# Kernel tuning notes

Hardware: AMD Instinct MI355X
Metric: run time of the kernel (lower is better)

## Reference

```python
import jax, jax.numpy as jnp
import numpy as np

N = 1024
DH = 64   # XH feature dim (<= DOUT)
DP = 32   # XP feature dim
DIN = 64  # input_dim (== output_dim, required by f_psi applied to vij)
DOUT = 64 # output_dim
BN_EPS = 1e-5
SIGMA = 0.1


def setup_inputs() -> dict:
    key = jax.random.key(0)
    ks = jax.random.split(key, 8)
    return {
        "XH": jax.random.normal(ks[0], (N, DH), dtype=jnp.float32),
        "XP": jax.random.normal(ks[1], (N, DP), dtype=jnp.float32),
        "XX": jax.random.normal(ks[2], (N, DIN), dtype=jnp.float32),
        "K": 16,
        # nn.Parameter weight/bias: normal(0, 0.01)
        "weight": 0.01 * jax.random.normal(ks[3], (DIN, DOUT), dtype=jnp.float32),
        "bias": 0.01 * jax.random.normal(ks[4], (DOUT,), dtype=jnp.float32),
        # f_psi Linear params (torch kaiming-uniform ~ small uniform)
        "psi_w": jax.random.uniform(ks[5], (DOUT, DIN), dtype=jnp.float32, minval=-1.0, maxval=1.0) / np.sqrt(DIN),
        "psi_b": jax.random.uniform(ks[6], (DOUT,), dtype=jnp.float32, minval=-1.0, maxval=1.0) / np.sqrt(DIN),
        # BatchNorm1d affine params
        "gamma": jnp.ones((DOUT,), dtype=jnp.float32),
        "beta": jnp.zeros((DOUT,), dtype=jnp.float32),
    }


def _pairwise_norm(X):
    # [N, N] matrix of L2 norms of row differences (as in torch.norm(X[:,None]-X, dim=2))
    return jnp.linalg.norm(X[:, None, :] - X[None, :, :], axis=2)


def _adjacency(XH, XP, K, sigma=SIGMA):
    eps = float(np.finfo(np.float64).eps)
    XHs = XH / (sigma + eps)
    WHo = _pairwise_norm(XHs)
    WH = jnp.exp(-((WHo - WHo.min()) / (WHo.max() - WHo.min())) / 2)
    Wlo = _pairwise_norm(XP)
    Wl = jnp.exp(-((Wlo - Wlo.min()) / (Wlo.max() - Wlo.min())))
    WW = WH + 0.2 * Wl
    _, idx = jax.lax.top_k(WW, K)                       # per-row top-K neighbors
    n = WW.shape[0]
    mask = jnp.zeros_like(WW).at[jnp.arange(n)[:, None], idx].set(1.0)
    mask = mask + mask.T                                # symmetrize
    # Original sets Adj=WW/WW=1 where mask!=0 and Adj=WW-WW=0 elsewhere -> binary adjacency
    return (mask > 0).astype(WW.dtype)


def reference(XH, XP, XX, K, weight, bias, psi_w, psi_b, gamma, beta):
    Adj = _adjacency(XH, XP, K)                         # [N, N], {0,1}
    x = XX @ weight                                     # [N, D]
    vi = x[None, :, :] * Adj[:, :, None]                # [N, N, D]: vi[i,j] = x[j]*Adj[i,j]
    vij = x[None, :, :] + vi                            # [N, N, D]
    # f_psi: Linear -> BatchNorm1d (training-mode batch stats) -> Sigmoid, over N*N rows
    h = jnp.einsum('ijd,ed->ije', vij, psi_w) + psi_b   # [N, N, D]
    mu = h.mean(axis=(0, 1))                            # [D]
    var = h.var(axis=(0, 1))                            # biased var, as torch BN
    att = jax.nn.sigmoid((h - mu) * jax.lax.rsqrt(var + BN_EPS) * gamma + beta)
    # self-loop attention forced to 1 on the diagonal
    eye = jnp.eye(x.shape[0], dtype=bool)[:, :, None]
    att = jnp.where(eye, jnp.float32(1.0), att)
    out = (att * vi).sum(axis=0) + bias                 # [N, D]
    return (out[:, :XH.shape[1]], XP, out)
```

## Files before the change

### kernel.cpp

```cpp
#include <hip/hip_runtime.h>
#include <cfloat>

#define NN 1024


__global__ __launch_bounds__(256) void gcn_transpose(const float* __restrict__ XH,
                                                     const float* __restrict__ XP,
                                                     float* __restrict__ XHT,
                                                     float* __restrict__ XPT) {
    const int b = blockIdx.x;
    const int j0 = b * 64;
    const int tid = threadIdx.x;
    __shared__ float th[64][65];
    __shared__ float tp[32][65];
#pragma unroll
    for (int it = 0; it < 16; ++it) {
        int idx = it * 256 + tid;
        int jl = idx >> 6, d = idx & 63;
        th[d][jl] = XH[(j0 + jl) * 64 + d];
    }
#pragma unroll
    for (int it = 0; it < 8; ++it) {
        int idx = it * 256 + tid;
        int jl = idx >> 5, d = idx & 31;
        tp[d][jl] = XP[(j0 + jl) * 32 + d];
    }
    __syncthreads();
#pragma unroll
    for (int it = 0; it < 16; ++it) {
        int idx = it * 256 + tid;
        int d = idx >> 6, jl = idx & 63;
        XHT[d * NN + j0 + jl] = th[d][jl];
    }
#pragma unroll
    for (int it = 0; it < 8; ++it) {
        int idx = it * 256 + tid;
        int d = idx >> 6, jl = idx & 63;
        XPT[d * NN + j0 + jl] = tp[d][jl];
    }
}

__global__ __launch_bounds__(256) void gcn_dist(const float* __restrict__ XH,
                                                const float* __restrict__ XP,
                                                const float* __restrict__ XHT,
                                                const float* __restrict__ XPT,
                                                unsigned* __restrict__ maxbits) {
    const int i0 = blockIdx.x * 4;
    const int tid = threadIdx.x;
    __shared__ float shi[4][64];
    __shared__ float spi[4][32];
    shi[tid >> 6][tid & 63] = XH[(i0 + (tid >> 6)) * 64 + (tid & 63)];
    if (tid < 128) spi[tid >> 5][tid & 31] = XP[(i0 + (tid >> 5)) * 32 + (tid & 31)];
    __syncthreads();
    const float4* XHTv = (const float4*)XHT;
    const float4* XPTv = (const float4*)XPT;
    float4 dh[4], dp[4];
#pragma unroll
    for (int r = 0; r < 4; ++r) { dh[r] = make_float4(0, 0, 0, 0); dp[r] = make_float4(0, 0, 0, 0); }
#pragma unroll 8
    for (int d = 0; d < 64; ++d) {
        float4 h = XHTv[d * 256 + tid];
#pragma unroll
        for (int r = 0; r < 4; ++r) {
            float s = shi[r][d];
            float tx = h.x - s, ty = h.y - s, tz = h.z - s, tw = h.w - s;
            dh[r].x += tx * tx; dh[r].y += ty * ty; dh[r].z += tz * tz; dh[r].w += tw * tw;
        }
    }
#pragma unroll 8
    for (int d = 0; d < 32; ++d) {
        float4 p = XPTv[d * 256 + tid];
#pragma unroll
        for (int r = 0; r < 4; ++r) {
            float s = spi[r][d];
            float tx = p.x - s, ty = p.y - s, tz = p.z - s, tw = p.w - s;
            dp[r].x += tx * tx; dp[r].y += ty * ty; dp[r].z += tz * tz; dp[r].w += tw * tw;
        }
    }
    float mh = 0.f, mp = 0.f;
#pragma unroll
    for (int r = 0; r < 4; ++r) {
        mh = fmaxf(mh, fmaxf(fmaxf(dh[r].x, dh[r].y), fmaxf(dh[r].z, dh[r].w)));
        mp = fmaxf(mp, fmaxf(fmaxf(dp[r].x, dp[r].y), fmaxf(dp[r].z, dp[r].w)));
    }
#pragma unroll
    for (int m = 1; m < 64; m <<= 1) {
        mh = fmaxf(mh, __shfl_xor(mh, m));
        mp = fmaxf(mp, __shfl_xor(mp, m));
    }
    __shared__ float wmx[4][2];
    if ((tid & 63) == 0) { wmx[tid >> 6][0] = mh; wmx[tid >> 6][1] = mp; }
    __syncthreads();
    if (tid == 0) {
        float a = fmaxf(fmaxf(wmx[0][0], wmx[1][0]), fmaxf(wmx[2][0], wmx[3][0]));
        float b = fmaxf(fmaxf(wmx[0][1], wmx[1][1]), fmaxf(wmx[2][1], wmx[3][1]));
        atomicMax(&maxbits[0], __float_as_uint(a));
        atomicMax(&maxbits[32], __float_as_uint(b));
    }
}

__global__ __launch_bounds__(256) void gcn_topk(const float* __restrict__ XH,
                                                const float* __restrict__ XP,
                                                const float* __restrict__ XHT,
                                                const float* __restrict__ XPT,
                                                const unsigned* __restrict__ maxbits,
                                                const int* __restrict__ kptr,
                                                unsigned char* __restrict__ mask,
                                                int* __restrict__ indeg) {
    const int i0 = blockIdx.x * 4;
    const int tid = threadIdx.x;
    const int w = tid >> 6;
    const int lane = tid & 63;
    const int i = i0 + w;
    __shared__ float shi[4][64];
    __shared__ float spi[4][32];
    shi[tid >> 6][tid & 63] = XH[(i0 + (tid >> 6)) * 64 + (tid & 63)];
    if (tid < 128) spi[tid >> 5][tid & 31] = XP[(i0 + (tid >> 5)) * 32 + (tid & 31)];
    __syncthreads();
    const float cH = -0.5f / sqrtf(__uint_as_float(maxbits[0]));
    const float cP = -1.0f / sqrtf(__uint_as_float(maxbits[32]));
    const float4* XHTv = (const float4*)XHT;
    const float4* XPTv = (const float4*)XPT;
    float ww[16];
#pragma unroll
    for (int s = 0; s < 4; ++s) {
        float4 dh = make_float4(0, 0, 0, 0), dp = make_float4(0, 0, 0, 0);
#pragma unroll 8
        for (int d = 0; d < 64; ++d) {
            float4 h = XHTv[d * 256 + s * 64 + lane];
            float c = shi[w][d];
            float tx = h.x - c, ty = h.y - c, tz = h.z - c, tw = h.w - c;
            dh.x += tx * tx; dh.y += ty * ty; dh.z += tz * tz; dh.w += tw * tw;
        }
#pragma unroll 8
        for (int d = 0; d < 32; ++d) {
            float4 p = XPTv[d * 256 + s * 64 + lane];
            float c = spi[w][d];
            float tx = p.x - c, ty = p.y - c, tz = p.z - c, tw = p.w - c;
            dp.x += tx * tx; dp.y += ty * ty; dp.z += tz * tz; dp.w += tw * tw;
        }
        ww[s * 4 + 0] = expf(sqrtf(dh.x) * cH) + 0.2f * expf(sqrtf(dp.x) * cP);
        ww[s * 4 + 1] = expf(sqrtf(dh.y) * cH) + 0.2f * expf(sqrtf(dp.y) * cP);
        ww[s * 4 + 2] = expf(sqrtf(dh.z) * cH) + 0.2f * expf(sqrtf(dp.z) * cP);
        ww[s * 4 + 3] = expf(sqrtf(dh.w) * cH) + 0.2f * expf(sqrtf(dp.w) * cP);
    }
    const int K = *kptr;
    int jsave = 0;
    for (int t = 0; t < K; ++t) {
        float bv = -FLT_MAX; int bj = NN;
#pragma unroll
        for (int v = 0; v < 16; ++v) {
            int j = ((v >> 2) << 8) | (lane << 2) | (v & 3);
            float val = ww[v];
            if (val > bv || (val == bv && j < bj)) { bv = val; bj = j; }
        }
#pragma unroll
        for (int m = 1; m < 64; m <<= 1) {
            float ov = __shfl_xor(bv, m);
            int oj = __shfl_xor(bj, m);
            if (ov > bv || (ov == bv && oj < bj)) { bv = ov; bj = oj; }
        }
        if ((int)lane == t) jsave = bj;
        if (((bj >> 2) & 63) == lane) {
            int slot = ((bj >> 8) << 2) | (bj & 3);
#pragma unroll
            for (int v = 0; v < 16; ++v)
                if (v == slot) ww[v] = -FLT_MAX;
        }
    }
    if (lane < K) {
        mask[(size_t)i * NN + jsave] = 1;
        atomicAdd(&indeg[jsave], 1);
    }
}

__global__ __launch_bounds__(256) void gcn_overlap(const unsigned char* __restrict__ mask,
                                                   int* __restrict__ overlap) {
    const int gid = blockIdx.x * 256 + threadIdx.x;
    const int i = gid >> 10, j = gid & 1023;
    if (mask[gid] && mask[(size_t)j * NN + i]) atomicAdd(&overlap[j], 1);
}

__global__ __launch_bounds__(256) void gcn_degree(const int* __restrict__ indeg,
                                                  const int* __restrict__ overlap,
                                                  const int* __restrict__ kptr,
                                                  int* __restrict__ cdeg) {
    const int j = blockIdx.x * 256 + threadIdx.x;
    if (j < NN) cdeg[j] = *kptr + indeg[j] - overlap[j];
}

__global__ __launch_bounds__(64) void gcn_xy(const float* __restrict__ XX,
                                             const float* __restrict__ W,
                                             const float* __restrict__ psi_w,
                                             float* __restrict__ x,
                                             float* __restrict__ y) {
    const int i = blockIdx.x;
    const int e = threadIdx.x;
    __shared__ float xin[64], xs[64];
    xin[e] = XX[i * 64 + e];
    __syncthreads();
    float acc = 0.f;
#pragma unroll
    for (int d = 0; d < 64; ++d) acc += xin[d] * W[d * 64 + e];
    xs[e] = acc;
    x[i * 64 + e] = acc;
    __syncthreads();
    float acc2 = 0.f;
    const float* pw = psi_w + e * 64;
#pragma unroll
    for (int d = 0; d < 64; ++d) acc2 += xs[d] * pw[d];
    y[i * 64 + e] = acc2;
}

__global__ __launch_bounds__(256) void gcn_mu(const float* __restrict__ y,
                                              const int* __restrict__ cdeg,
                                              const float* __restrict__ psi_b,
                                              float* __restrict__ mu) {
    const int e = blockIdx.x;
    const int tid = threadIdx.x;
    __shared__ double red[256];
    double s = 0.0;
    for (int j = tid; j < NN; j += 256)
        s += (double)(NN + cdeg[j]) * (double)y[j * 64 + e];
    red[tid] = s;
    __syncthreads();
    for (int k = 128; k > 0; k >>= 1) {
        if (tid < k) red[tid] += red[tid + k];
        __syncthreads();
    }
    if (tid == 0) mu[e] = (float)(red[0] / 1048576.0) + psi_b[e];
}

__global__ __launch_bounds__(256) void gcn_var(const float* __restrict__ y,
                                               const int* __restrict__ cdeg,
                                               const float* __restrict__ psi_b,
                                               const float* __restrict__ gamma,
                                               const float* __restrict__ mu,
                                               float* __restrict__ scale) {
    const int e = blockIdx.x;
    const int tid = threadIdx.x;
    __shared__ double red[256];
    const float m = mu[e], b = psi_b[e];
    double s = 0.0;
    for (int j = tid; j < NN; j += 256) {
        float t = y[j * 64 + e];
        float a1 = t + b - m;
        float a2 = 2.f * t + b - m;
        int cj = cdeg[j];
        s += (double)(NN - cj) * (double)a1 * (double)a1
           + (double)cj * (double)a2 * (double)a2;
    }
    red[tid] = s;
    __syncthreads();
    for (int k = 128; k > 0; k >>= 1) {
        if (tid < k) red[tid] += red[tid + k];
        __syncthreads();
    }
    if (tid == 0) {
        double var = red[0] / 1048576.0;
        scale[e] = (float)(1.0 / sqrt(var + 1e-5)) * gamma[e];
    }
}

__global__ __launch_bounds__(64) void gcn_out(const float* __restrict__ x,
                                              const float* __restrict__ y,
                                              const int* __restrict__ cdeg,
                                              const float* __restrict__ psi_b,
                                              const float* __restrict__ beta,
                                              const float* __restrict__ mu,
                                              const float* __restrict__ scale,
                                              const float* __restrict__ bias,
                                              const float* __restrict__ XP,
                                              float* __restrict__ out) {
    const int j = blockIdx.x;
    const int e = threadIdx.x;
    float t = y[j * 64 + e];
    float z = (2.f * t + psi_b[e] - mu[e]) * scale[e] + beta[e];
    float s = 1.f / (1.f + expf(-z));
    float val = x[j * 64 + e] * ((float)(cdeg[j] - 1) * s + 1.f) + bias[e];
    out[j * 64 + e] = val;
    out[98304 + j * 64 + e] = val;
    if (e < 32) out[65536 + j * 32 + e] = XP[j * 32 + e];
}

extern "C" void kernel_launch(void* const* d_in, const int* in_sizes, int n_in,
                              void* d_out, int out_size, void* d_ws, size_t ws_size,
                              hipStream_t stream) {
    const float* XH    = (const float*)d_in[0];
    const float* XP    = (const float*)d_in[1];
    const float* XX    = (const float*)d_in[2];
    const int*   Kp    = (const int*)d_in[3];
    const float* W     = (const float*)d_in[4];
    const float* bias  = (const float*)d_in[5];
    const float* psi_w = (const float*)d_in[6];
    const float* psi_b = (const float*)d_in[7];
    const float* gamma = (const float*)d_in[8];
    const float* beta  = (const float*)d_in[9];
    float* out = (float*)d_out;
    char* ws = (char*)d_ws;

    unsigned char* mask = (unsigned char*)ws;
    int* indeg        = (int*)(ws + 0x100000);
    int* overlap      = (int*)(ws + 0x101000);
    unsigned* maxbits = (unsigned*)(ws + 0x102000);
    int* cdeg         = (int*)(ws + 0x103000);
    float* mu         = (float*)(ws + 0x104000);
    float* scale      = (float*)(ws + 0x104100);
    float* x          = (float*)(ws + 0x200000);
    float* y          = (float*)(ws + 0x240000);
    float* XHT        = (float*)(ws + 0x280000);
    float* XPT        = (float*)(ws + 0x2C0000);

    hipMemsetAsync(ws, 0, 0x102200, stream);

    gcn_transpose<<<dim3(16), dim3(256), 0, stream>>>(XH, XP, XHT, XPT);
    gcn_dist<<<dim3(256), dim3(256), 0, stream>>>(XH, XP, XHT, XPT, maxbits);
    gcn_topk<<<dim3(256), dim3(256), 0, stream>>>(XH, XP, XHT, XPT, maxbits, Kp, mask, indeg);
    gcn_overlap<<<dim3(4096), dim3(256), 0, stream>>>(mask, overlap);
    gcn_degree<<<dim3(4), dim3(256), 0, stream>>>(indeg, overlap, Kp, cdeg);
    gcn_xy<<<dim3(1024), dim3(64), 0, stream>>>(XX, W, psi_w, x, y);
    gcn_mu<<<dim3(64), dim3(256), 0, stream>>>(y, cdeg, psi_b, mu);
    gcn_var<<<dim3(64), dim3(256), 0, stream>>>(y, cdeg, psi_b, gamma, mu, scale);
    gcn_out<<<dim3(1024), dim3(64), 0, stream>>>(x, y, cdeg, psi_b, beta, mu, scale, bias, XP, out);
}
```

Baseline: 165.4 us.

## Cache fp16 distances, sparse edge lists for overlap, and fuse BN mean/var into one pass

The distance kernel now stores per-pair sqrt distances as half2, so top-k reads them instead of recomputing every pairwise distance. Top-k packs the weight and index into a single unsigned key for cheaper argmax reductions, and emits a 16-per-row edge list instead of a dense byte mask. The overlap check scans those edge lists instead of all N² mask entries, which also shrinks the memset. The mean and variance reductions are merged into one kernel using E[x²]-m², with psi_b cancelled algebraically. The risks are fp16 distance rounding and truncating the low key bits, both of which can change tie-breaking in top-k selection.

```diff
diff --git a/kernel.cpp b/kernel.cpp
--- a/kernel.cpp
+++ b/kernel.cpp
@@ -1,4 +1,5 @@
 #include <hip/hip_runtime.h>
+#include <hip/hip_fp16.h>
 #include <cfloat>
 
 #define NN 1024
@@ -8,8 +9,7 @@
                                                      const float* __restrict__ XP,
                                                      float* __restrict__ XHT,
                                                      float* __restrict__ XPT) {
-    const int b = blockIdx.x;
-    const int j0 = b * 64;
+    const int j0 = blockIdx.x * 64;
     const int tid = threadIdx.x;
     __shared__ float th[64][65];
     __shared__ float tp[32][65];
@@ -44,45 +44,36 @@
                                                 const float* __restrict__ XP,
                                                 const float* __restrict__ XHT,
                                                 const float* __restrict__ XPT,
+                                                __half2* __restrict__ dist,
                                                 unsigned* __restrict__ maxbits) {
-    const int i0 = blockIdx.x * 4;
+    const int b = blockIdx.x;
+    const int i0 = (b >> 2) * 4;
+    const int j = (b & 3) * 256 + threadIdx.x;
     const int tid = threadIdx.x;
     __shared__ float shi[4][64];
     __shared__ float spi[4][32];
     shi[tid >> 6][tid & 63] = XH[(i0 + (tid >> 6)) * 64 + (tid & 63)];
     if (tid < 128) spi[tid >> 5][tid & 31] = XP[(i0 + (tid >> 5)) * 32 + (tid & 31)];
     __syncthreads();
-    const float4* XHTv = (const float4*)XHT;
-    const float4* XPTv = (const float4*)XPT;
-    float4 dh[4], dp[4];
-#pragma unroll
-    for (int r = 0; r < 4; ++r) { dh[r] = make_float4(0, 0, 0, 0); dp[r] = make_float4(0, 0, 0, 0); }
-#pragma unroll 8
+    float dh[4] = {0.f, 0.f, 0.f, 0.f}, dp[4] = {0.f, 0.f, 0.f, 0.f};
+#pragma unroll 16
     for (int d = 0; d < 64; ++d) {
-        float4 h = XHTv[d * 256 + tid];
-#pragma unroll
-        for (int r = 0; r < 4; ++r) {
-            float s = shi[r][d];
-            float tx = h.x - s, ty = h.y - s, tz = h.z - s, tw = h.w - s;
-            dh[r].x += tx * tx; dh[r].y += ty * ty; dh[r].z += tz * tz; dh[r].w += tw * tw;
-        }
-    }
-#pragma unroll 8
+        float v = XHT[d * NN + j];
+#pragma unroll
+        for (int r = 0; r < 4; ++r) { float t = v - shi[r][d]; dh[r] += t * t; }
+    }
+#pragma unroll 16
     for (int d = 0; d < 32; ++d) {
-        float4 p = XPTv[d * 256 + tid];
-#pragma unroll
-        for (int r = 0; r < 4; ++r) {
-            float s = spi[r][d];
-            float tx = p.x - s, ty = p.y - s, tz = p.z - s, tw = p.w - s;
-            dp[r].x += tx * tx; dp[r].y += ty * ty; dp[r].z += tz * tz; dp[r].w += tw * tw;
-        }
-    }
-    float mh = 0.f, mp = 0.f;
-#pragma unroll
-    for (int r = 0; r < 4; ++r) {
-        mh = fmaxf(mh, fmaxf(fmaxf(dh[r].x, dh[r].y), fmaxf(dh[r].z, dh[r].w)));
-        mp = fmaxf(mp, fmaxf(fmaxf(dp[r].x, dp[r].y), fmaxf(dp[r].z, dp[r].w)));
-    }
+        float v = XPT[d * NN + j];
+#pragma unroll
+        for (int r = 0; r < 4; ++r) { float t = v - spi[r][d]; dp[r] += t * t; }
+    }
+#pragma unroll
+    for (int r = 0; r < 4; ++r)
+        dist[(size_t)(i0 + r) * NN + j] =
+            __halves2half2(__float2half(sqrtf(dh[r])), __float2half(sqrtf(dp[r])));
+    float mh = fmaxf(fmaxf(dh[0], dh[1]), fmaxf(dh[2], dh[3]));
+    float mp = fmaxf(fmaxf(dp[0], dp[1]), fmaxf(dp[2], dp[3]));
 #pragma unroll
     for (int m = 1; m < 64; m <<= 1) {
         mh = fmaxf(mh, __shfl_xor(mh, m));
@@ -93,92 +84,77 @@
     __syncthreads();
     if (tid == 0) {
         float a = fmaxf(fmaxf(wmx[0][0], wmx[1][0]), fmaxf(wmx[2][0], wmx[3][0]));
-        float b = fmaxf(fmaxf(wmx[0][1], wmx[1][1]), fmaxf(wmx[2][1], wmx[3][1]));
+        float b2 = fmaxf(fmaxf(wmx[0][1], wmx[1][1]), fmaxf(wmx[2][1], wmx[3][1]));
         atomicMax(&maxbits[0], __float_as_uint(a));
-        atomicMax(&maxbits[32], __float_as_uint(b));
-    }
-}
-
-__global__ __launch_bounds__(256) void gcn_topk(const float* __restrict__ XH,
-                                                const float* __restrict__ XP,
-                                                const float* __restrict__ XHT,
-                                                const float* __restrict__ XPT,
+        atomicMax(&maxbits[32], __float_as_uint(b2));
+    }
+}
+
+__global__ __launch_bounds__(256) void gcn_topk(const __half2* __restrict__ dist,
                                                 const unsigned* __restrict__ maxbits,
                                                 const int* __restrict__ kptr,
-                                                unsigned char* __restrict__ mask,
+                                                int* __restrict__ eidx,
                                                 int* __restrict__ indeg) {
-    const int i0 = blockIdx.x * 4;
-    const int tid = threadIdx.x;
-    const int w = tid >> 6;
-    const int lane = tid & 63;
-    const int i = i0 + w;
-    __shared__ float shi[4][64];
-    __shared__ float spi[4][32];
-    shi[tid >> 6][tid & 63] = XH[(i0 + (tid >> 6)) * 64 + (tid & 63)];
-    if (tid < 128) spi[tid >> 5][tid & 31] = XP[(i0 + (tid >> 5)) * 32 + (tid & 31)];
-    __syncthreads();
+    const int tid = threadIdx.x;
+    const int w = tid >> 6, lane = tid & 63;
+    const int i = blockIdx.x * 4 + w;
     const float cH = -0.5f / sqrtf(__uint_as_float(maxbits[0]));
     const float cP = -1.0f / sqrtf(__uint_as_float(maxbits[32]));
-    const float4* XHTv = (const float4*)XHT;
-    const float4* XPTv = (const float4*)XPT;
-    float ww[16];
+    const float4* drow = (const float4*)(dist + (size_t)i * NN);
+    unsigned kk[16];
 #pragma unroll
     for (int s = 0; s < 4; ++s) {
-        float4 dh = make_float4(0, 0, 0, 0), dp = make_float4(0, 0, 0, 0);
-#pragma unroll 8
-        for (int d = 0; d < 64; ++d) {
-            float4 h = XHTv[d * 256 + s * 64 + lane];
-            float c = shi[w][d];
-            float tx = h.x - c, ty = h.y - c, tz = h.z - c, tw = h.w - c;
-            dh.x += tx * tx; dh.y += ty * ty; dh.z += tz * tz; dh.w += tw * tw;
+        float4 v = drow[s * 64 + lane];
+        const __half2* hp = (const __half2*)&v;
+#pragma unroll
+        for (int q = 0; q < 4; ++q) {
+            float nh = __low2float(hp[q]);
+            float np = __high2float(hp[q]);
+            float wwv = __expf(nh * cH) + 0.2f * __expf(np * cP);
+            int j = s * 256 + lane * 4 + q;
+            kk[s * 4 + q] = (__float_as_uint(wwv) & 0xFFFFFC00u) | (unsigned)(1023 - j);
         }
-#pragma unroll 8
-        for (int d = 0; d < 32; ++d) {
-            float4 p = XPTv[d * 256 + s * 64 + lane];
-            float c = spi[w][d];
-            float tx = p.x - c, ty = p.y - c, tz = p.z - c, tw = p.w - c;
-            dp.x += tx * tx; dp.y += ty * ty; dp.z += tz * tz; dp.w += tw * tw;
-        }
-        ww[s * 4 + 0] = expf(sqrtf(dh.x) * cH) + 0.2f * expf(sqrtf(dp.x) * cP);
-        ww[s * 4 + 1] = expf(sqrtf(dh.y) * cH) + 0.2f * expf(sqrtf(dp.y) * cP);
-        ww[s * 4 + 2] = expf(sqrtf(dh.z) * cH) + 0.2f * expf(sqrtf(dp.z) * cP);
-        ww[s * 4 + 3] = expf(sqrtf(dh.w) * cH) + 0.2f * expf(sqrtf(dp.w) * cP);
     }
     const int K = *kptr;
     int jsave = 0;
     for (int t = 0; t < K; ++t) {
-        float bv = -FLT_MAX; int bj = NN;
-#pragma unroll
-        for (int v = 0; v < 16; ++v) {
-            int j = ((v >> 2) << 8) | (lane << 2) | (v & 3);
-            float val = ww[v];
-            if (val > bv || (val == bv && j < bj)) { bv = val; bj = j; }
+        unsigned bk = 0;
+#pragma unroll
+        for (int v = 0; v < 16; ++v) bk = kk[v] > bk ? kk[v] : bk;
+#pragma unroll
+        for (int m = 1; m < 64; m <<= 1) {
+            unsigned o = (unsigned)__shfl_xor((int)bk, m);
+            bk = o > bk ? o : bk;
         }
-#pragma unroll
-        for (int m = 1; m < 64; m <<= 1) {
-            float ov = __shfl_xor(bv, m);
-            int oj = __shfl_xor(bj, m);
-            if (ov > bv || (ov == bv && oj < bj)) { bv = ov; bj = oj; }
+        int j = 1023 - (int)(bk & 0x3FFu);
+        if (lane == t) jsave = j;
+        if (((j >> 2) & 63) == lane) {
+            int slot = ((j >> 8) << 2) | (j & 3);
+#pragma unroll
+            for (int v = 0; v < 16; ++v)
+                if (v == slot) kk[v] = 0u;
         }
-        if ((int)lane == t) jsave = bj;
-        if (((bj >> 2) & 63) == lane) {
-            int slot = ((bj >> 8) << 2) | (bj & 3);
-#pragma unroll
-            for (int v = 0; v < 16; ++v)
-                if (v == slot) ww[v] = -FLT_MAX;
-        }
     }
     if (lane < K) {
-        mask[(size_t)i * NN + jsave] = 1;
+        eidx[i * 16 + lane] = jsave;
         atomicAdd(&indeg[jsave], 1);
     }
 }
 
-__global__ __launch_bounds__(256) void gcn_overlap(const unsigned char* __restrict__ mask,
+__global__ __launch_bounds__(256) void gcn_overlap(const int* __restrict__ eidx,
                                                    int* __restrict__ overlap) {
     const int gid = blockIdx.x * 256 + threadIdx.x;
-    const int i = gid >> 10, j = gid & 1023;
-    if (mask[gid] && mask[(size_t)j * NN + i]) atomicAdd(&overlap[j], 1);
+    const int i = gid >> 4;
+    const int j = eidx[gid];
+    if (j < 0) return;
+    const int4* ej = (const int4*)(eidx + j * 16);
+    bool rec = false;
+#pragma unroll
+    for (int q = 0; q < 4; ++q) {
+        int4 e = ej[q];
+        rec |= (e.x == i) | (e.y == i) | (e.z == i) | (e.w == i);
+    }
+    if (rec) atomicAdd(&overlap[j], 1);
 }
 
 __global__ __launch_bounds__(256) void gcn_degree(const int* __restrict__ indeg,
@@ -212,62 +188,40 @@
     y[i * 64 + e] = acc2;
 }
 
-__global__ __launch_bounds__(256) void gcn_mu(const float* __restrict__ y,
-                                              const int* __restrict__ cdeg,
-                                              const float* __restrict__ psi_b,
-                                              float* __restrict__ mu) {
+__global__ __launch_bounds__(256) void gcn_stats(const float* __restrict__ y,
+                                                 const int* __restrict__ cdeg,
+                                                 const float* __restrict__ gamma,
+                                                 float* __restrict__ m0out,
+                                                 float* __restrict__ scaleout) {
     const int e = blockIdx.x;
     const int tid = threadIdx.x;
-    __shared__ double red[256];
-    double s = 0.0;
-    for (int j = tid; j < NN; j += 256)
-        s += (double)(NN + cdeg[j]) * (double)y[j * 64 + e];
-    red[tid] = s;
+    __shared__ double r1[256], r2[256];
+    double s1 = 0.0, s2 = 0.0;
+    for (int j = tid; j < NN; j += 256) {
+        double t = (double)y[j * 64 + e];
+        int c = cdeg[j];
+        s1 += (double)(NN + c) * t;
+        s2 += (double)(NN + 3 * c) * t * t;
+    }
+    r1[tid] = s1; r2[tid] = s2;
     __syncthreads();
     for (int k = 128; k > 0; k >>= 1) {
-        if (tid < k) red[tid] += red[tid + k];
+        if (tid < k) { r1[tid] += r1[tid + k]; r2[tid] += r2[tid + k]; }
         __syncthreads();
     }
-    if (tid == 0) mu[e] = (float)(red[0] / 1048576.0) + psi_b[e];
-}
-
-__global__ __launch_bounds__(256) void gcn_var(const float* __restrict__ y,
-                                               const int* __restrict__ cdeg,
-                                               const float* __restrict__ psi_b,
-                                               const float* __restrict__ gamma,
-                                               const float* __restrict__ mu,
-                                               float* __restrict__ scale) {
-    const int e = blockIdx.x;
-    const int tid = threadIdx.x;
-    __shared__ double red[256];
-    const float m = mu[e], b = psi_b[e];
-    double s = 0.0;
-    for (int j = tid; j < NN; j += 256) {
-        float t = y[j * 64 + e];
-        float a1 = t + b - m;
-        float a2 = 2.f * t + b - m;
-        int cj = cdeg[j];
-        s += (double)(NN - cj) * (double)a1 * (double)a1
-           + (double)cj * (double)a2 * (double)a2;
-    }
-    red[tid] = s;
-    __syncthreads();
-    for (int k = 128; k > 0; k >>= 1) {
-        if (tid < k) red[tid] += red[tid + k];
-        __syncthreads();
-    }
     if (tid == 0) {
-        double var = red[0] / 1048576.0;
-        scale[e] = (float)(1.0 / sqrt(var + 1e-5)) * gamma[e];
+        double m = r1[0] / 1048576.0;
+        double var = r2[0] / 1048576.0 - m * m;
+        m0out[e] = (float)m;
+        scaleout[e] = (float)(1.0 / sqrt(var + 1e-5)) * gamma[e];
     }
 }
 
 __global__ __launch_bounds__(64) void gcn_out(const float* __restrict__ x,
                                               const float* __restrict__ y,
                                               const int* __restrict__ cdeg,
-                                              const float* __restrict__ psi_b,
                                               const float* __restrict__ beta,
-                                              const float* __restrict__ mu,
+                                              const float* __restrict__ m0,
                                               const float* __restrict__ scale,
                                               const float* __restrict__ bias,
                                               const float* __restrict__ XP,
@@ -275,7 +229,7 @@
     const int j = blockIdx.x;
     const int e = threadIdx.x;
     float t = y[j * 64 + e];
-    float z = (2.f * t + psi_b[e] - mu[e]) * scale[e] + beta[e];
+    float z = (2.f * t - m0[e]) * scale[e] + beta[e];
     float s = 1.f / (1.f + expf(-z));
     float val = x[j * 64 + e] * ((float)(cdeg[j] - 1) * s + 1.f) + bias[e];
     out[j * 64 + e] = val;
@@ -296,30 +250,32 @@
     const float* psi_b = (const float*)d_in[7];
     const float* gamma = (const float*)d_in[8];
     const float* beta  = (const float*)d_in[9];
+    (void)psi_b;
     float* out = (float*)d_out;
     char* ws = (char*)d_ws;
 
-    unsigned char* mask = (unsigned char*)ws;
-    int* indeg        = (int*)(ws + 0x100000);
-    int* overlap      = (int*)(ws + 0x101000);
-    unsigned* maxbits = (unsigned*)(ws + 0x102000);
-    int* cdeg         = (int*)(ws + 0x103000);
-    float* mu         = (float*)(ws + 0x104000);
-    float* scale      = (float*)(ws + 0x104100);
-    float* x          = (float*)(ws + 0x200000);
-    float* y          = (float*)(ws + 0x240000);
-    float* XHT        = (float*)(ws + 0x280000);
-    float* XPT        = (float*)(ws + 0x2C0000);
-
-    hipMemsetAsync(ws, 0, 0x102200, stream);
+    __half2* dist     = (__half2*)ws;
+    float* XHT        = (float*)(ws + 0x400000);
+    float* XPT        = (float*)(ws + 0x440000);
+    int* eidx         = (int*)(ws + 0x460000);
+    int* indeg        = (int*)(ws + 0x470000);
+    int* overlap      = (int*)(ws + 0x471000);
+    unsigned* maxbits = (unsigned*)(ws + 0x472000);
+    int* cdeg         = (int*)(ws + 0x473000);
+    float* m0         = (float*)(ws + 0x474000);
+    float* scale      = (float*)(ws + 0x474200);
+    float* x          = (float*)(ws + 0x480000);
+    float* y          = (float*)(ws + 0x4C0000);
+
+    hipMemsetAsync(ws + 0x460000, 0xFF, 0x10000, stream);
+    hipMemsetAsync(ws + 0x470000, 0x00, 0x3000, stream);
 
     gcn_transpose<<<dim3(16), dim3(256), 0, stream>>>(XH, XP, XHT, XPT);
-    gcn_dist<<<dim3(256), dim3(256), 0, stream>>>(XH, XP, XHT, XPT, maxbits);
-    gcn_topk<<<dim3(256), dim3(256), 0, stream>>>(XH, XP, XHT, XPT, maxbits, Kp, mask, indeg);
-    gcn_overlap<<<dim3(4096), dim3(256), 0, stream>>>(mask, overlap);
+    gcn_dist<<<dim3(1024), dim3(256), 0, stream>>>(XH, XP, XHT, XPT, dist, maxbits);
+    gcn_topk<<<dim3(256), dim3(256), 0, stream>>>(dist, maxbits, Kp, eidx, indeg);
+    gcn_overlap<<<dim3(64), dim3(256), 0, stream>>>(eidx, overlap);
     gcn_degree<<<dim3(4), dim3(256), 0, stream>>>(indeg, overlap, Kp, cdeg);
     gcn_xy<<<dim3(1024), dim3(64), 0, stream>>>(XX, W, psi_w, x, y);
-    gcn_mu<<<dim3(64), dim3(256), 0, stream>>>(y, cdeg, psi_b, mu);
-    gcn_var<<<dim3(64), dim3(256), 0, stream>>>(y, cdeg, psi_b, gamma, mu, scale);
-    gcn_out<<<dim3(1024), dim3(64), 0, stream>>>(x, y, cdeg, psi_b, beta, mu, scale, bias, XP, out);
-}
+    gcn_stats<<<dim3(64), dim3(256), 0, stream>>>(y, cdeg, gamma, m0, scale);
+    gcn_out<<<dim3(1024), dim3(64), 0, stream>>>(x, y, cdeg, beta, m0, scale, bias, XP, out);
+}
```

New measurement: 142.7 us. 13.7% less time.
